# Performance work log

Hardware: AMD Instinct MI355X
Metric: run time of the kernel (lower is better)

The kernel has to match this reference:

```python
import jax, jax.numpy as jnp
import numpy as np

N_EMBD = 1024
D_FF = 4096
N_EXPERTS = 8
TOP_K = 2


def setup_inputs() -> dict:
    key = jax.random.key(0)
    k1, k2, k3, k4 = jax.random.split(key, 4)
    x = jax.random.normal(k1, (1, 2048, N_EMBD), dtype=jnp.float32)
    mask = jnp.ones((2048, N_EXPERTS), dtype=jnp.float32)
    Wr = jax.random.normal(k2, (N_EMBD, N_EXPERTS), dtype=jnp.float32) * 0.02
    W1 = jax.random.normal(k3, (N_EXPERTS, N_EMBD, D_FF), dtype=jnp.float32) * 0.02
    W2 = jax.random.normal(k4, (N_EXPERTS, D_FF, N_EMBD), dtype=jnp.float32) * 0.02
    return {"x": x, "mask": mask, "Wr": Wr, "W1": W1, "W2": W2}


def reference(x, mask, Wr, W1, W2):
    T = x.shape[0] * x.shape[1]
    xs = x.reshape(T, N_EMBD)                      # [T, d]
    router_logits = (xs @ Wr) * mask               # [T, E], masked as in MaskedMoE
    all_probs = jax.nn.softmax(router_logits, axis=-1)  # softmax_topk order
    weights, selected = jax.lax.top_k(all_probs, TOP_K)  # [T, K]
    # combine[t, e] = sum of routing weights where token t selected expert e
    combine = jnp.zeros((T, N_EXPERTS), dtype=xs.dtype)
    combine = combine.at[jnp.arange(T)[:, None], selected].add(weights)
    results = jnp.zeros_like(xs)
    for e in range(N_EXPERTS):  # fixed small expert count
        h = jax.nn.gelu(xs @ W1[e])                # [T, d_ff]
        out = h @ W2[e]                            # [T, d]
        results = results + combine[:, e:e + 1] * out
    return results.reshape(x.shape)
```

## Files before the change

kernel.cpp:

```cpp
#include <hip/hip_runtime.h>
#include <hip/hip_bf16.h>


#define T_TOK 2048
#define D_EMB 1024
#define DFF   4096
#define NE    8

typedef _Float16 f16x8 __attribute__((ext_vector_type(8)));
typedef float    f32x4 __attribute__((ext_vector_type(4)));

__device__ __forceinline__ float gelu_tanh(float x) {
    const float c = 0.7978845608028654f;
    float z = c * (x + 0.044715f * x * x * x);
    float u = __expf(2.0f * z);
    return 0.5f * x * (1.0f + (u - 1.0f) / (u + 1.0f));
}

__device__ __forceinline__ void gll(const void* g, void* l) {
    __builtin_amdgcn_global_load_lds((__attribute__((address_space(1))) void*)g,
                                     (__attribute__((address_space(3))) void*)l,
                                     16, 0, 0);
}

__global__ void k_zero(int* counts) {
    if (threadIdx.x < NE) counts[threadIdx.x] = 0;
}

__global__ __launch_bounds__(256) void k_router(
    const float* __restrict__ x, const float* __restrict__ mask,
    const float* __restrict__ Wr, _Float16* __restrict__ xh,
    int* __restrict__ counts, int* __restrict__ elist,
    int* __restrict__ tok_e, int* __restrict__ tok_p, float* __restrict__ tok_w) {
    int wave = threadIdx.x >> 6;
    int lane = threadIdx.x & 63;
    int t = blockIdx.x * 4 + wave;
    if (t >= T_TOK) return;

    float acc[NE];
#pragma unroll
    for (int e = 0; e < NE; e++) acc[e] = 0.f;
    const float* xr = x + (size_t)t * D_EMB;
    for (int c = 0; c < D_EMB / 64; c++) {
        int i = c * 64 + lane;
        float xv = xr[i];
        xh[(size_t)t * D_EMB + i] = (_Float16)xv;
        const float* wr = Wr + (size_t)i * NE;
#pragma unroll
        for (int e = 0; e < NE; e++) acc[e] += xv * wr[e];
    }
#pragma unroll
    for (int e = 0; e < NE; e++) {
#pragma unroll
        for (int off = 32; off > 0; off >>= 1)
            acc[e] += __shfl_xor(acc[e], off);
    }
    if (lane == 0) {
        float p[NE];
        float mx = -1e30f;
#pragma unroll
        for (int e = 0; e < NE; e++) {
            p[e] = acc[e] * mask[t * NE + e];
            mx = fmaxf(mx, p[e]);
        }
        float s = 0.f;
#pragma unroll
        for (int e = 0; e < NE; e++) { p[e] = expf(p[e] - mx); s += p[e]; }
#pragma unroll
        for (int e = 0; e < NE; e++) p[e] /= s;
        int e0 = 0; float b0 = p[0];
#pragma unroll
        for (int e = 1; e < NE; e++) if (p[e] > b0) { b0 = p[e]; e0 = e; }
        int e1 = -1; float b1 = -1.f;
#pragma unroll
        for (int e = 0; e < NE; e++) if (e != e0 && p[e] > b1) { b1 = p[e]; e1 = e; }

        int pos0 = atomicAdd(&counts[e0], 1);
        elist[e0 * T_TOK + pos0] = t;
        tok_e[t * 2 + 0] = e0; tok_p[t * 2 + 0] = pos0; tok_w[t * 2 + 0] = b0;
        int pos1 = atomicAdd(&counts[e1], 1);
        elist[e1 * T_TOK + pos1] = t;
        tok_e[t * 2 + 1] = e1; tok_p[t * 2 + 1] = pos1; tok_w[t * 2 + 1] = b1;
    }
}

__global__ __launch_bounds__(256) void k_transpose(
    const float* __restrict__ W1, const float* __restrict__ W2,
    _Float16* __restrict__ W1T, _Float16* __restrict__ W2T) {
    int bz = blockIdx.z;
    int e = bz & 7;
    bool isW2 = bz >= 8;
    const float* S = (isW2 ? W2 : W1) + (size_t)e * 4194304;
    _Float16* Dst = (isW2 ? W2T : W1T) + (size_t)e * 4194304;
    int ld      = isW2 ? 1024 : 4096;
    int ktplane = isW2 ? 65536 : 262144;
    int bx = blockIdx.x;
    int g, nb;
    if (isW2) { g = bx; nb = 0; }
    else      { g = bx >> 2; nb = (bx & 3) * 1024; }

    int t = threadIdx.x;
    int n = nb + t * 4;
    const float* src = S + (size_t)(g * 8) * ld + n;

    f32x4 v[8];
#pragma unroll
    for (int r = 0; r < 8; r++)
        v[r] = *(const f32x4*)(src + (size_t)r * ld);

    f16x8 o[4];
#pragma unroll
    for (int j = 0; j < 4; j++)
#pragma unroll
        for (int u = 0; u < 8; u++)
            o[j][u] = (_Float16)v[u][j];

    size_t off = (size_t)(g >> 3) * ktplane + (size_t)(n >> 7) * 8192
               + (g & 7) * 1024 + (n & 127) * 8;
    f16x8* d = (f16x8*)(Dst + off);
#pragma unroll
    for (int j = 0; j < 4; j++) d[j] = o[j];
}


__global__ __launch_bounds__(256) void k_gemm1(
    const _Float16* __restrict__ xh, const _Float16* __restrict__ BT,
    const int* __restrict__ counts, const int* __restrict__ elist,
    _Float16* __restrict__ H) {
    int e = blockIdx.z;
    int cnt = counts[e];
    int p0 = blockIdx.y * 128;
    if (p0 >= cnt) return;
    int rowbase = 0;
    for (int i = 0; i < NE; i++) rowbase += (i < e) ? counts[i] : 0;
    int n0 = blockIdx.x * 128;
    const _Float16* B = BT + (size_t)e * 4194304;

    __shared__ _Float16 As[128 * 64];
    __shared__ _Float16 Bs[128 * 64];
    __shared__ int ttok[128];

    int tid = threadIdx.x;
    if (tid < 128) ttok[tid] = elist[e * T_TOK + min(p0 + tid, cnt - 1)];
    __syncthreads();

    int w = tid >> 6, lane = tid & 63;
    int rq = tid >> 3;
    int cch = (tid & 7) ^ ((tid >> 3) & 7);
    const _Float16* pA[4];
    const _Float16* pB[4];
    _Float16* lA[4];
    _Float16* lB[4];
#pragma unroll
    for (int q = 0; q < 4; q++) {
        int row = q * 32 + rq;
        pA[q] = xh + (size_t)ttok[row] * D_EMB + cch * 8;
        pB[q] = B + (size_t)n0 * 64 + (q * 256 + tid) * 8;
        lA[q] = As + (q * 256 + w * 64) * 8;
        lB[q] = Bs + (q * 256 + w * 64) * 8;
    }

    int wm = w >> 1, wn = w & 1;
    int lhi = lane >> 4, llo = lane & 15;
    int m7 = llo & 7;
    int kc0 = lhi ^ m7, kc1 = kc0 ^ 4;
    const _Float16* arp0 = As + (wm * 64 + llo) * 64 + kc0 * 8;
    const _Float16* arp1 = As + (wm * 64 + llo) * 64 + kc1 * 8;
    const _Float16* brp0 = Bs + (lhi * 128 + wn * 64 + llo) * 8;
    const _Float16* brp1 = Bs + ((lhi + 4) * 128 + wn * 64 + llo) * 8;

    f32x4 acc[4][4] = {};
    for (int it = 0; it < 16; ++it) {
        __syncthreads();
#pragma unroll
        for (int q = 0; q < 4; q++) { gll(pA[q], lA[q]); gll(pB[q], lB[q]); }
#pragma unroll
        for (int q = 0; q < 4; q++) { pA[q] += 64; pB[q] += 262144; }
        __syncthreads();
        f16x8 a[4], b[4];
#pragma unroll
        for (int i = 0; i < 4; i++) {
            a[i] = *(const f16x8*)(arp0 + i * 1024);
            b[i] = *(const f16x8*)(brp0 + i * 128);
        }
#pragma unroll
        for (int mt = 0; mt < 4; mt++)
#pragma unroll
            for (int nt = 0; nt < 4; nt++)
                acc[mt][nt] = __builtin_amdgcn_mfma_f32_16x16x32_f16(a[mt], b[nt], acc[mt][nt], 0, 0, 0);
#pragma unroll
        for (int i = 0; i < 4; i++) {
            a[i] = *(const f16x8*)(arp1 + i * 1024);
            b[i] = *(const f16x8*)(brp1 + i * 128);
        }
#pragma unroll
        for (int mt = 0; mt < 4; mt++)
#pragma unroll
            for (int nt = 0; nt < 4; nt++)
                acc[mt][nt] = __builtin_amdgcn_mfma_f32_16x16x32_f16(a[mt], b[nt], acc[mt][nt], 0, 0, 0);
    }

#pragma unroll
    for (int mt = 0; mt < 4; mt++) {
#pragma unroll
        for (int i = 0; i < 4; i++) {
            int p = p0 + wm * 64 + mt * 16 + lhi * 4 + i;
            if (p < cnt) {
                size_t rowoff = (size_t)(rowbase + p) * DFF + n0 + wn * 64 + llo;
#pragma unroll
                for (int nt = 0; nt < 4; nt++)
                    H[rowoff + nt * 16] = (_Float16)gelu_tanh(acc[mt][nt][i]);
            }
        }
    }
}

__global__ __launch_bounds__(256) void k_gemm2(
    const _Float16* __restrict__ H, const _Float16* __restrict__ BT,
    const int* __restrict__ counts, float* __restrict__ Obase) {
    int bz = blockIdx.z;
    int e = bz & 7, sp = bz >> 3;
    int cnt = counts[e];
    int p0 = blockIdx.y * 128;
    if (p0 >= cnt) return;
    int rowbase = 0;
    for (int i = 0; i < NE; i++) rowbase += (i < e) ? counts[i] : 0;
    int n0 = blockIdx.x * 128;
    int kh = sp * 1024;
    const _Float16* B = BT + (size_t)e * 4194304;
    float* O = Obase + (size_t)sp * 4194304;

    __shared__ _Float16 As[128 * 64];
    __shared__ _Float16 Bs[128 * 64];

    int tid = threadIdx.x;
    int w = tid >> 6, lane = tid & 63;
    int rq = tid >> 3;
    int cch = (tid & 7) ^ ((tid >> 3) & 7);
    const _Float16* pA[4];
    const _Float16* pB[4];
    _Float16* lA[4];
    _Float16* lB[4];
#pragma unroll
    for (int q = 0; q < 4; q++) {
        int row = q * 32 + rq;
        int r = rowbase + min(p0 + row, cnt - 1);
        pA[q] = H + (size_t)r * DFF + kh + cch * 8;
        pB[q] = B + (size_t)(sp * 16) * 65536 + (size_t)n0 * 64 + (q * 256 + tid) * 8;
        lA[q] = As + (q * 256 + w * 64) * 8;
        lB[q] = Bs + (q * 256 + w * 64) * 8;
    }

    int wm = w >> 1, wn = w & 1;
    int lhi = lane >> 4, llo = lane & 15;
    int m7 = llo & 7;
    int kc0 = lhi ^ m7, kc1 = kc0 ^ 4;
    const _Float16* arp0 = As + (wm * 64 + llo) * 64 + kc0 * 8;
    const _Float16* arp1 = As + (wm * 64 + llo) * 64 + kc1 * 8;
    const _Float16* brp0 = Bs + (lhi * 128 + wn * 64 + llo) * 8;
    const _Float16* brp1 = Bs + ((lhi + 4) * 128 + wn * 64 + llo) * 8;

    f32x4 acc[4][4] = {};
    for (int it = 0; it < 16; ++it) {
        __syncthreads();
#pragma unroll
        for (int q = 0; q < 4; q++) { gll(pA[q], lA[q]); gll(pB[q], lB[q]); }
#pragma unroll
        for (int q = 0; q < 4; q++) { pA[q] += 64; pB[q] += 65536; }
        __syncthreads();
        f16x8 a[4], b[4];
#pragma unroll
        for (int i = 0; i < 4; i++) {
            a[i] = *(const f16x8*)(arp0 + i * 1024);
            b[i] = *(const f16x8*)(brp0 + i * 128);
        }
#pragma unroll
        for (int mt = 0; mt < 4; mt++)
#pragma unroll
            for (int nt = 0; nt < 4; nt++)
                acc[mt][nt] = __builtin_amdgcn_mfma_f32_16x16x32_f16(a[mt], b[nt], acc[mt][nt], 0, 0, 0);
#pragma unroll
        for (int i = 0; i < 4; i++) {
            a[i] = *(const f16x8*)(arp1 + i * 1024);
            b[i] = *(const f16x8*)(brp1 + i * 128);
        }
#pragma unroll
        for (int mt = 0; mt < 4; mt++)
#pragma unroll
            for (int nt = 0; nt < 4; nt++)
                acc[mt][nt] = __builtin_amdgcn_mfma_f32_16x16x32_f16(a[mt], b[nt], acc[mt][nt], 0, 0, 0);
    }

#pragma unroll
    for (int mt = 0; mt < 4; mt++) {
#pragma unroll
        for (int i = 0; i < 4; i++) {
            int p = p0 + wm * 64 + mt * 16 + lhi * 4 + i;
            if (p < cnt) {
                size_t o = (size_t)(rowbase + p) * D_EMB + n0 + wn * 64 + llo;
#pragma unroll
                for (int nt = 0; nt < 4; nt++)
                    O[o + nt * 16] = acc[mt][nt][i];
            }
        }
    }
}

__global__ __launch_bounds__(256) void k_final(
    const float* __restrict__ Obase, const int* __restrict__ counts,
    const int* __restrict__ tok_e, const int* __restrict__ tok_p,
    const float* __restrict__ tok_w, float* __restrict__ out) {
    __shared__ int sb[NE];
    int t = blockIdx.x;
    if (threadIdx.x == 0) {
        int s = 0;
        for (int e = 0; e < NE; e++) { sb[e] = s; s += counts[e]; }
    }
    __syncthreads();
    int r0 = sb[tok_e[t * 2 + 0]] + tok_p[t * 2 + 0];
    int r1 = sb[tok_e[t * 2 + 1]] + tok_p[t * 2 + 1];
    float w0 = tok_w[t * 2 + 0], w1 = tok_w[t * 2 + 1];
    int i = threadIdx.x * 4;
    float4 s0 = {0, 0, 0, 0}, s1 = {0, 0, 0, 0};
#pragma unroll
    for (int sp = 0; sp < 4; sp++) {
        const float* O = Obase + (size_t)sp * 4194304;
        float4 a = *(const float4*)(O + (size_t)r0 * D_EMB + i);
        float4 b = *(const float4*)(O + (size_t)r1 * D_EMB + i);
        s0.x += a.x; s0.y += a.y; s0.z += a.z; s0.w += a.w;
        s1.x += b.x; s1.y += b.y; s1.z += b.z; s1.w += b.w;
    }
    float4 o;
    o.x = w0 * s0.x + w1 * s1.x;
    o.y = w0 * s0.y + w1 * s1.y;
    o.z = w0 * s0.z + w1 * s1.z;
    o.w = w0 * s0.w + w1 * s1.w;
    *(float4*)(out + (size_t)t * D_EMB + i) = o;
}

extern "C" void kernel_launch(void* const* d_in, const int* in_sizes, int n_in,
                              void* d_out, int out_size, void* d_ws, size_t ws_size,
                              hipStream_t stream) {
    const float* x    = (const float*)d_in[0];
    const float* mask = (const float*)d_in[1];
    const float* Wr   = (const float*)d_in[2];
    const float* W1   = (const float*)d_in[3];
    const float* W2   = (const float*)d_in[4];
    float* out = (float*)d_out;

    char* ws = (char*)d_ws;
    const size_t MB = 1024 * 1024;
    int*      counts = (int*)(ws + 0);
    int*      elist  = (int*)(ws + 1024);
    int*      tok_e  = (int*)(ws + 1024 + 65536);
    int*      tok_p  = (int*)(ws + 1024 + 65536 + 16384);
    float*    tok_w  = (float*)(ws + 1024 + 65536 + 32768);
    _Float16* xh     = (_Float16*)(ws + 1 * MB);
    _Float16* W1T    = (_Float16*)(ws + 8 * MB);
    _Float16* W2T    = (_Float16*)(ws + 72 * MB);
    _Float16* H      = (_Float16*)(ws + 136 * MB);
    float*    Obuf   = (float*)(ws + 168 * MB);

    k_zero<<<1, 64, 0, stream>>>(counts);
    k_router<<<T_TOK / 4, 256, 0, stream>>>(x, mask, Wr, xh, counts, elist, tok_e, tok_p, tok_w);
    k_transpose<<<dim3(512, 1, 16), 256, 0, stream>>>(W1, W2, W1T, W2T);
    k_gemm1<<<dim3(32, 16, NE), 256, 0, stream>>>(xh, W1T, counts, elist, H);
    k_gemm2<<<dim3(8, 16, 32), 256, 0, stream>>>(H, W2T, counts, Obuf);
    k_final<<<T_TOK, 256, 0, stream>>>(Obuf, counts, tok_e, tok_p, tok_w, out);
}
```

Baseline: 504.7 us.

## Overlap weight transposes with router and first GEMM via fused launches

The standalone transpose kernel is split up. The W1 transpose now runs as extra blocks in the router kernel, and the W2 transpose is interleaved block-by-block with the first expert GEMM in a single 1D grid. The goal is to remove a launch and let the bandwidth-bound weight conversion run alongside compute-bound GEMM work instead of serially. The cost is index decoding in a flattened grid, and the GEMM blocks may lose some cache locality or occupancy because they share the device with transpose traffic.

```diff
diff --git a/kernel.cpp b/kernel.cpp
--- a/kernel.cpp
+++ b/kernel.cpp
@@ -27,15 +27,45 @@
     if (threadIdx.x < NE) counts[threadIdx.x] = 0;
 }
 
-__global__ __launch_bounds__(256) void k_router(
+__device__ __forceinline__ void transpose_body(
+    const float* __restrict__ S, _Float16* __restrict__ Dst,
+    int ld, int ktplane, int g, int nb, int tid) {
+    int n = nb + tid * 4;
+    const float* src = S + (size_t)(g * 8) * ld + n;
+    f32x4 v[8];
+#pragma unroll
+    for (int r = 0; r < 8; r++)
+        v[r] = *(const f32x4*)(src + (size_t)r * ld);
+    f16x8 o[4];
+#pragma unroll
+    for (int j = 0; j < 4; j++)
+#pragma unroll
+        for (int u = 0; u < 8; u++)
+            o[j][u] = (_Float16)v[u][j];
+    size_t off = (size_t)(g >> 3) * ktplane + (size_t)(n >> 7) * 8192
+               + (g & 7) * 1024 + (n & 127) * 8;
+    f16x8* d = (f16x8*)(Dst + off);
+#pragma unroll
+    for (int j = 0; j < 4; j++) d[j] = o[j];
+}
+
+__global__ __launch_bounds__(256) void k_f1(
     const float* __restrict__ x, const float* __restrict__ mask,
     const float* __restrict__ Wr, _Float16* __restrict__ xh,
     int* __restrict__ counts, int* __restrict__ elist,
-    int* __restrict__ tok_e, int* __restrict__ tok_p, float* __restrict__ tok_w) {
+    int* __restrict__ tok_e, int* __restrict__ tok_p, float* __restrict__ tok_w,
+    const float* __restrict__ W1, _Float16* __restrict__ W1T) {
+    int bid = blockIdx.x;
+    if (bid >= 512) {
+        int idx = bid - 512;
+        int e = idx >> 9, bx = idx & 511;
+        transpose_body(W1 + (size_t)e * 4194304, W1T + (size_t)e * 4194304,
+                       4096, 262144, bx >> 2, (bx & 3) * 1024, threadIdx.x);
+        return;
+    }
     int wave = threadIdx.x >> 6;
     int lane = threadIdx.x & 63;
-    int t = blockIdx.x * 4 + wave;
-    if (t >= T_TOK) return;
+    int t = bid * 4 + wave;
 
     float acc[NE];
 #pragma unroll
@@ -84,63 +114,35 @@
     }
 }
 
-__global__ __launch_bounds__(256) void k_transpose(
-    const float* __restrict__ W1, const float* __restrict__ W2,
-    _Float16* __restrict__ W1T, _Float16* __restrict__ W2T) {
-    int bz = blockIdx.z;
-    int e = bz & 7;
-    bool isW2 = bz >= 8;
-    const float* S = (isW2 ? W2 : W1) + (size_t)e * 4194304;
-    _Float16* Dst = (isW2 ? W2T : W1T) + (size_t)e * 4194304;
-    int ld      = isW2 ? 1024 : 4096;
-    int ktplane = isW2 ? 65536 : 262144;
-    int bx = blockIdx.x;
-    int g, nb;
-    if (isW2) { g = bx; nb = 0; }
-    else      { g = bx >> 2; nb = (bx & 3) * 1024; }
-
-    int t = threadIdx.x;
-    int n = nb + t * 4;
-    const float* src = S + (size_t)(g * 8) * ld + n;
-
-    f32x4 v[8];
-#pragma unroll
-    for (int r = 0; r < 8; r++)
-        v[r] = *(const f32x4*)(src + (size_t)r * ld);
-
-    f16x8 o[4];
-#pragma unroll
-    for (int j = 0; j < 4; j++)
-#pragma unroll
-        for (int u = 0; u < 8; u++)
-            o[j][u] = (_Float16)v[u][j];
-
-    size_t off = (size_t)(g >> 3) * ktplane + (size_t)(n >> 7) * 8192
-               + (g & 7) * 1024 + (n & 127) * 8;
-    f16x8* d = (f16x8*)(Dst + off);
-#pragma unroll
-    for (int j = 0; j < 4; j++) d[j] = o[j];
-}
-
-
-__global__ __launch_bounds__(256) void k_gemm1(
+
+__global__ __launch_bounds__(256) void k_f2(
     const _Float16* __restrict__ xh, const _Float16* __restrict__ BT,
     const int* __restrict__ counts, const int* __restrict__ elist,
-    _Float16* __restrict__ H) {
-    int e = blockIdx.z;
+    _Float16* __restrict__ H,
+    const float* __restrict__ W2, _Float16* __restrict__ W2T) {
+    int bid = blockIdx.x;
+    int tid = threadIdx.x;
+    if (bid & 1) {
+        int idx = bid >> 1;
+        int e = idx >> 9, bx = idx & 511;
+        transpose_body(W2 + (size_t)e * 4194304, W2T + (size_t)e * 4194304,
+                       1024, 65536, bx, 0, tid);
+        return;
+    }
+    int gid = bid >> 1;
+    int e = gid >> 9;
     int cnt = counts[e];
-    int p0 = blockIdx.y * 128;
+    int p0 = ((gid >> 5) & 15) * 128;
     if (p0 >= cnt) return;
     int rowbase = 0;
     for (int i = 0; i < NE; i++) rowbase += (i < e) ? counts[i] : 0;
-    int n0 = blockIdx.x * 128;
+    int n0 = (gid & 31) * 128;
     const _Float16* B = BT + (size_t)e * 4194304;
 
     __shared__ _Float16 As[128 * 64];
     __shared__ _Float16 Bs[128 * 64];
     __shared__ int ttok[128];
 
-    int tid = threadIdx.x;
     if (tid < 128) ttok[tid] = elist[e * T_TOK + min(p0 + tid, cnt - 1)];
     __syncthreads();
 
@@ -362,9 +364,9 @@
     float*    Obuf   = (float*)(ws + 168 * MB);
 
     k_zero<<<1, 64, 0, stream>>>(counts);
-    k_router<<<T_TOK / 4, 256, 0, stream>>>(x, mask, Wr, xh, counts, elist, tok_e, tok_p, tok_w);
-    k_transpose<<<dim3(512, 1, 16), 256, 0, stream>>>(W1, W2, W1T, W2T);
-    k_gemm1<<<dim3(32, 16, NE), 256, 0, stream>>>(xh, W1T, counts, elist, H);
+    k_f1<<<512 + 4096, 256, 0, stream>>>(x, mask, Wr, xh, counts, elist,
+                                         tok_e, tok_p, tok_w, W1, W1T);
+    k_f2<<<8192, 256, 0, stream>>>(xh, W1T, counts, elist, H, W2, W2T);
     k_gemm2<<<dim3(8, 16, 32), 256, 0, stream>>>(H, W2T, counts, Obuf);
     k_final<<<T_TOK, 256, 0, stream>>>(Obuf, counts, tok_e, tok_p, tok_w, out);
 }
```

New measurement: 499.3 us. About the same (-1.1%).

## Fuse fp32 weight conversion into expert GEMMs and remap blocks per XCD

Applied to the files above, without the earlier changes.

Removes the separate transpose kernel that converted W1/W2 to fp16 in a blocked layout. Each GEMM block now loads fp32 weights directly, converts them in registers and writes them to swizzled LDS, so the fp16 weight copies are no longer written to and re-read from global memory. Launch grids are flattened to 1D with an index remap that groups blocks sharing the same weight column tile onto the same XCD for L2 reuse. The trade-off is that each block reloads and reconverts fp32 weights, doubling weight bytes per load. The B loads are also now synchronous register loads instead of async global-to-LDS loads.

```diff
diff --git a/kernel.cpp b/kernel.cpp
--- a/kernel.cpp
+++ b/kernel.cpp
@@ -84,60 +84,26 @@
     }
 }
 
-__global__ __launch_bounds__(256) void k_transpose(
-    const float* __restrict__ W1, const float* __restrict__ W2,
-    _Float16* __restrict__ W1T, _Float16* __restrict__ W2T) {
-    int bz = blockIdx.z;
-    int e = bz & 7;
-    bool isW2 = bz >= 8;
-    const float* S = (isW2 ? W2 : W1) + (size_t)e * 4194304;
-    _Float16* Dst = (isW2 ? W2T : W1T) + (size_t)e * 4194304;
-    int ld      = isW2 ? 1024 : 4096;
-    int ktplane = isW2 ? 65536 : 262144;
-    int bx = blockIdx.x;
-    int g, nb;
-    if (isW2) { g = bx; nb = 0; }
-    else      { g = bx >> 2; nb = (bx & 3) * 1024; }
-
-    int t = threadIdx.x;
-    int n = nb + t * 4;
-    const float* src = S + (size_t)(g * 8) * ld + n;
-
-    f32x4 v[8];
-#pragma unroll
-    for (int r = 0; r < 8; r++)
-        v[r] = *(const f32x4*)(src + (size_t)r * ld);
-
-    f16x8 o[4];
-#pragma unroll
-    for (int j = 0; j < 4; j++)
-#pragma unroll
-        for (int u = 0; u < 8; u++)
-            o[j][u] = (_Float16)v[u][j];
-
-    size_t off = (size_t)(g >> 3) * ktplane + (size_t)(n >> 7) * 8192
-               + (g & 7) * 1024 + (n & 127) * 8;
-    f16x8* d = (f16x8*)(Dst + off);
-#pragma unroll
-    for (int j = 0; j < 4; j++) d[j] = o[j];
-}
-
 
 __global__ __launch_bounds__(256) void k_gemm1(
-    const _Float16* __restrict__ xh, const _Float16* __restrict__ BT,
+    const _Float16* __restrict__ xh, const float* __restrict__ W1,
     const int* __restrict__ counts, const int* __restrict__ elist,
     _Float16* __restrict__ H) {
-    int e = blockIdx.z;
+    int bid = blockIdx.x;
+    int xcd = bid & 7, local = bid >> 3;
+    int n0i = (xcd << 2) | (local >> 7);
+    int e   = (local >> 4) & 7;
+    int pt  = local & 15;
     int cnt = counts[e];
-    int p0 = blockIdx.y * 128;
+    int p0 = pt * 128;
     if (p0 >= cnt) return;
     int rowbase = 0;
     for (int i = 0; i < NE; i++) rowbase += (i < e) ? counts[i] : 0;
-    int n0 = blockIdx.x * 128;
-    const _Float16* B = BT + (size_t)e * 4194304;
+    int n0 = n0i * 128;
+    const float* Bsrc = W1 + (size_t)e * 4194304;
 
     __shared__ _Float16 As[128 * 64];
-    __shared__ _Float16 Bs[128 * 64];
+    __shared__ _Float16 Bs[8 * 128 * 8];
     __shared__ int ttok[128];
 
     int tid = threadIdx.x;
@@ -148,17 +114,21 @@
     int rq = tid >> 3;
     int cch = (tid & 7) ^ ((tid >> 3) & 7);
     const _Float16* pA[4];
-    const _Float16* pB[4];
     _Float16* lA[4];
-    _Float16* lB[4];
 #pragma unroll
     for (int q = 0; q < 4; q++) {
         int row = q * 32 + rq;
         pA[q] = xh + (size_t)ttok[row] * D_EMB + cch * 8;
-        pB[q] = B + (size_t)n0 * 64 + (q * 256 + tid) * 8;
         lA[q] = As + (q * 256 + w * 64) * 8;
-        lB[q] = Bs + (q * 256 + w * 64) * 8;
-    }
+    }
+
+    int g = tid >> 5, l5 = tid & 31;
+    const float* pB = Bsrc + (size_t)(g * 8) * 4096 + n0 + l5 * 4;
+    int xr = (l5 >> 1) & 7;
+    _Float16* wp[4];
+#pragma unroll
+    for (int j = 0; j < 4; j++)
+        wp[j] = Bs + g * 1024 + (((4 * l5 + j) ^ xr) * 8);
 
     int wm = w >> 1, wn = w & 1;
     int lhi = lane >> 4, llo = lane & 15;
@@ -166,22 +136,39 @@
     int kc0 = lhi ^ m7, kc1 = kc0 ^ 4;
     const _Float16* arp0 = As + (wm * 64 + llo) * 64 + kc0 * 8;
     const _Float16* arp1 = As + (wm * 64 + llo) * 64 + kc1 * 8;
-    const _Float16* brp0 = Bs + (lhi * 128 + wn * 64 + llo) * 8;
-    const _Float16* brp1 = Bs + ((lhi + 4) * 128 + wn * 64 + llo) * 8;
+    int bofs[4];
+#pragma unroll
+    for (int nt = 0; nt < 4; nt++) {
+        int n = wn * 64 + nt * 16 + llo;
+        bofs[nt] = lhi * 1024 + ((n ^ ((n >> 3) & 7)) * 8);
+    }
 
     f32x4 acc[4][4] = {};
     for (int it = 0; it < 16; ++it) {
         __syncthreads();
-#pragma unroll
-        for (int q = 0; q < 4; q++) { gll(pA[q], lA[q]); gll(pB[q], lB[q]); }
-#pragma unroll
-        for (int q = 0; q < 4; q++) { pA[q] += 64; pB[q] += 262144; }
+        f32x4 v[8];
+#pragma unroll
+        for (int r = 0; r < 8; r++)
+            v[r] = *(const f32x4*)(pB + (size_t)r * 4096);
+#pragma unroll
+        for (int q = 0; q < 4; q++) gll(pA[q], lA[q]);
+        f16x8 o[4];
+#pragma unroll
+        for (int j = 0; j < 4; j++)
+#pragma unroll
+            for (int u = 0; u < 8; u++)
+                o[j][u] = (_Float16)v[u][j];
+#pragma unroll
+        for (int j = 0; j < 4; j++) *(f16x8*)wp[j] = o[j];
+        pB += 64 * 4096;
+#pragma unroll
+        for (int q = 0; q < 4; q++) pA[q] += 64;
         __syncthreads();
         f16x8 a[4], b[4];
 #pragma unroll
         for (int i = 0; i < 4; i++) {
             a[i] = *(const f16x8*)(arp0 + i * 1024);
-            b[i] = *(const f16x8*)(brp0 + i * 128);
+            b[i] = *(const f16x8*)(Bs + bofs[i]);
         }
 #pragma unroll
         for (int mt = 0; mt < 4; mt++)
@@ -191,7 +178,7 @@
 #pragma unroll
         for (int i = 0; i < 4; i++) {
             a[i] = *(const f16x8*)(arp1 + i * 1024);
-            b[i] = *(const f16x8*)(brp1 + i * 128);
+            b[i] = *(const f16x8*)(Bs + bofs[i] + 4096);
         }
 #pragma unroll
         for (int mt = 0; mt < 4; mt++)
@@ -216,40 +203,47 @@
 }
 
 __global__ __launch_bounds__(256) void k_gemm2(
-    const _Float16* __restrict__ H, const _Float16* __restrict__ BT,
+    const _Float16* __restrict__ H, const float* __restrict__ W2,
     const int* __restrict__ counts, float* __restrict__ Obase) {
-    int bz = blockIdx.z;
-    int e = bz & 7, sp = bz >> 3;
+    int bid = blockIdx.x;
+    int xcd = bid & 7, local = bid >> 3;
+    int g2 = (xcd << 5) | (local >> 4);
+    int pt = local & 15;
+    int e = g2 & 7, sp = (g2 >> 3) & 3, n0i = g2 >> 5;
     int cnt = counts[e];
-    int p0 = blockIdx.y * 128;
+    int p0 = pt * 128;
     if (p0 >= cnt) return;
     int rowbase = 0;
     for (int i = 0; i < NE; i++) rowbase += (i < e) ? counts[i] : 0;
-    int n0 = blockIdx.x * 128;
+    int n0 = n0i * 128;
     int kh = sp * 1024;
-    const _Float16* B = BT + (size_t)e * 4194304;
+    const float* Bsrc = W2 + (size_t)e * 4194304;
     float* O = Obase + (size_t)sp * 4194304;
 
     __shared__ _Float16 As[128 * 64];
-    __shared__ _Float16 Bs[128 * 64];
+    __shared__ _Float16 Bs[8 * 128 * 8];
 
     int tid = threadIdx.x;
     int w = tid >> 6, lane = tid & 63;
     int rq = tid >> 3;
     int cch = (tid & 7) ^ ((tid >> 3) & 7);
     const _Float16* pA[4];
-    const _Float16* pB[4];
     _Float16* lA[4];
-    _Float16* lB[4];
 #pragma unroll
     for (int q = 0; q < 4; q++) {
         int row = q * 32 + rq;
         int r = rowbase + min(p0 + row, cnt - 1);
         pA[q] = H + (size_t)r * DFF + kh + cch * 8;
-        pB[q] = B + (size_t)(sp * 16) * 65536 + (size_t)n0 * 64 + (q * 256 + tid) * 8;
         lA[q] = As + (q * 256 + w * 64) * 8;
-        lB[q] = Bs + (q * 256 + w * 64) * 8;
-    }
+    }
+
+    int g = tid >> 5, l5 = tid & 31;
+    const float* pB = Bsrc + (size_t)(kh + g * 8) * 1024 + n0 + l5 * 4;
+    int xr = (l5 >> 1) & 7;
+    _Float16* wp[4];
+#pragma unroll
+    for (int j = 0; j < 4; j++)
+        wp[j] = Bs + g * 1024 + (((4 * l5 + j) ^ xr) * 8);
 
     int wm = w >> 1, wn = w & 1;
     int lhi = lane >> 4, llo = lane & 15;
@@ -257,22 +251,39 @@
     int kc0 = lhi ^ m7, kc1 = kc0 ^ 4;
     const _Float16* arp0 = As + (wm * 64 + llo) * 64 + kc0 * 8;
     const _Float16* arp1 = As + (wm * 64 + llo) * 64 + kc1 * 8;
-    const _Float16* brp0 = Bs + (lhi * 128 + wn * 64 + llo) * 8;
-    const _Float16* brp1 = Bs + ((lhi + 4) * 128 + wn * 64 + llo) * 8;
+    int bofs[4];
+#pragma unroll
+    for (int nt = 0; nt < 4; nt++) {
+        int n = wn * 64 + nt * 16 + llo;
+        bofs[nt] = lhi * 1024 + ((n ^ ((n >> 3) & 7)) * 8);
+    }
 
     f32x4 acc[4][4] = {};
     for (int it = 0; it < 16; ++it) {
         __syncthreads();
-#pragma unroll
-        for (int q = 0; q < 4; q++) { gll(pA[q], lA[q]); gll(pB[q], lB[q]); }
-#pragma unroll
-        for (int q = 0; q < 4; q++) { pA[q] += 64; pB[q] += 65536; }
+        f32x4 v[8];
+#pragma unroll
+        for (int r = 0; r < 8; r++)
+            v[r] = *(const f32x4*)(pB + (size_t)r * 1024);
+#pragma unroll
+        for (int q = 0; q < 4; q++) gll(pA[q], lA[q]);
+        f16x8 o[4];
+#pragma unroll
+        for (int j = 0; j < 4; j++)
+#pragma unroll
+            for (int u = 0; u < 8; u++)
+                o[j][u] = (_Float16)v[u][j];
+#pragma unroll
+        for (int j = 0; j < 4; j++) *(f16x8*)wp[j] = o[j];
+        pB += 64 * 1024;
+#pragma unroll
+        for (int q = 0; q < 4; q++) pA[q] += 64;
         __syncthreads();
         f16x8 a[4], b[4];
 #pragma unroll
         for (int i = 0; i < 4; i++) {
             a[i] = *(const f16x8*)(arp0 + i * 1024);
-            b[i] = *(const f16x8*)(brp0 + i * 128);
+            b[i] = *(const f16x8*)(Bs + bofs[i]);
         }
 #pragma unroll
         for (int mt = 0; mt < 4; mt++)
@@ -282,7 +293,7 @@
 #pragma unroll
         for (int i = 0; i < 4; i++) {
             a[i] = *(const f16x8*)(arp1 + i * 1024);
-            b[i] = *(const f16x8*)(brp1 + i * 128);
+            b[i] = *(const f16x8*)(Bs + bofs[i] + 4096);
         }
 #pragma unroll
         for (int mt = 0; mt < 4; mt++)
@@ -356,15 +367,12 @@
     int*      tok_p  = (int*)(ws + 1024 + 65536 + 16384);
     float*    tok_w  = (float*)(ws + 1024 + 65536 + 32768);
     _Float16* xh     = (_Float16*)(ws + 1 * MB);
-    _Float16* W1T    = (_Float16*)(ws + 8 * MB);
-    _Float16* W2T    = (_Float16*)(ws + 72 * MB);
-    _Float16* H      = (_Float16*)(ws + 136 * MB);
-    float*    Obuf   = (float*)(ws + 168 * MB);
+    _Float16* H      = (_Float16*)(ws + 8 * MB);
+    float*    Obuf   = (float*)(ws + 40 * MB);
 
     k_zero<<<1, 64, 0, stream>>>(counts);
     k_router<<<T_TOK / 4, 256, 0, stream>>>(x, mask, Wr, xh, counts, elist, tok_e, tok_p, tok_w);
-    k_transpose<<<dim3(512, 1, 16), 256, 0, stream>>>(W1, W2, W1T, W2T);
-    k_gemm1<<<dim3(32, 16, NE), 256, 0, stream>>>(xh, W1T, counts, elist, H);
-    k_gemm2<<<dim3(8, 16, 32), 256, 0, stream>>>(H, W2T, counts, Obuf);
+    k_gemm1<<<4096, 256, 0, stream>>>(xh, W1, counts, elist, H);
+    k_gemm2<<<4096, 256, 0, stream>>>(H, W2, counts, Obuf);
     k_final<<<T_TOK, 256, 0, stream>>>(Obuf, counts, tok_e, tok_p, tok_w, out);
 }
```

Result: faster. 473.7 us (-6.1%).
